# Kernel optimization log

Hardware: AMD Instinct MI355X
Metric: run time of the kernel (lower is better)

Reference implementation:

```python
import jax, jax.numpy as jnp
import numpy as np

T, D, E, K = 16384, 4096, 64, 8
GUMBEL_TAU = 1.0
ROUTER_TEMP = 1.0
SELECT_TEMP = None  # falls back to router_temp, as in the module
EPS = 1e-06


def setup_inputs() -> dict:
    key = jax.random.key(0)
    k1, k2, k3 = jax.random.split(key, 3)
    h = jax.random.normal(k1, (T, D), dtype=jnp.float32)
    # eqx.nn.Linear weight: shape (out_features, in_features), uniform init scale
    W = jax.random.normal(k2, (E, D), dtype=jnp.float32) * (1.0 / np.sqrt(D))
    # uniform noise for Gumbel, matching minval=1e-6, maxval=1-1e-6
    u = jax.random.uniform(k3, (T, E), minval=EPS, maxval=1.0 - EPS, dtype=jnp.float32)
    return {"h": h, "W": W, "u": u}


def reference(h, W, u):
    # logits_clean = vmap(Linear)(h) = h @ W.T, shape (T, E)
    logits_clean = jnp.einsum("td,ed->te", h, W)

    t_mix = jnp.clip(jnp.float32(ROUTER_TEMP), EPS, None)
    probs = jax.nn.softmax(logits_clean / t_mix, axis=-1)

    sel_temp = ROUTER_TEMP if SELECT_TEMP is None else SELECT_TEMP
    t_sel = jnp.clip(jnp.float32(sel_temp), EPS, None)
    logits_sel = logits_clean / t_sel

    # training path: Gumbel noise g = -log(-log(u))
    g = -jnp.log(-jnp.log(u))
    logits_sel = logits_sel + GUMBEL_TAU * g

    # hard top-k mask per row (scatter of ones at top-k indices == one_hot().sum())
    _, idx = jax.lax.top_k(logits_sel, K)  # (T, K)
    rows = jnp.arange(logits_sel.shape[0])[:, None]
    mask_full = jnp.zeros(logits_sel.shape, dtype=bool).at[rows, idx].set(True)

    return (mask_full, probs, logits_clean, logits_sel)
```

## Files before the change

### kernel.cpp

```cpp
#include <hip/hip_runtime.h>
#include <hip/hip_bf16.h>
#include <math.h>
#include <stdint.h>

#define T_ROWS 16384
#define D_DIM  4096
#define E_EXP  64
#define TOPK   8

constexpr float W_SCALE   = 64.0f;
constexpr float INV_SCALE = 1.0f / 64.0f;

constexpr int BM   = 64;
constexpr int BK   = 32;
constexpr int KQ   = D_DIM / 4;
constexpr int NIT  = KQ / BK;
constexpr int ABUF = 8192;
constexpr int BBUF = 8192;
constexpr int B_OFF = 3 * ABUF;
constexpr int LDS_TOT = B_OFF + 2 * BBUF;

typedef _Float16 f16x8 __attribute__((ext_vector_type(8)));
typedef __fp16   h16x2 __attribute__((ext_vector_type(2)));
typedef float    f32x4 __attribute__((ext_vector_type(4)));

__device__ __forceinline__ void gll16(const void* g, void* l) {
    __builtin_amdgcn_global_load_lds(
        (const __attribute__((address_space(1))) void*)g,
        (__attribute__((address_space(3))) void*)l, 16, 0, 0);
}
#define WAITV(n) asm volatile("s_waitcnt vmcnt(" #n ")" ::: "memory")
#define SB0()    __builtin_amdgcn_sched_barrier(0)

__global__ __launch_bounds__(256) void wprep_kernel(
    const float* __restrict__ W, _Float16* __restrict__ Wt)
{
    const int i  = blockIdx.x * 256 + threadIdx.x;
    const int e  = i >> 9;
    const int k8 = i & 511;
    const int k  = k8 << 3;
    const int t  = k >> 5;
    const int s  = (k >> 3) & 3;
    const float4 w0 = *(const float4*)&W[(size_t)e * D_DIM + k];
    const float4 w1 = *(const float4*)&W[(size_t)e * D_DIM + k + 4];
    const float xs[8] = {w0.x, w0.y, w0.z, w0.w, w1.x, w1.y, w1.z, w1.w};
    f16x8 hi, lo;
    #pragma unroll
    for (int j = 0; j < 8; ++j) {
        const float x = xs[j] * W_SCALE;
        const _Float16 hh = (_Float16)x;
        hi[j] = hh;
        lo[j] = (_Float16)(x - (float)hh);
    }
    const size_t o = (size_t)t * 4096 + e * 32 + ((s ^ (e & 3)) << 3);
    *(f16x8*)(Wt + o) = hi;
    *(f16x8*)(Wt + o + 2048) = lo;
}

__device__ __forceinline__ void cvt8(const float4 x0, const float4 x1,
                                     f16x8& hi, f16x8& lo) {
    const float xs[8] = {x0.x, x0.y, x0.z, x0.w, x1.x, x1.y, x1.z, x1.w};
    float hs[8], ls[8];
    #pragma unroll
    for (int j = 0; j < 8; ++j) {
        hs[j] = __uint_as_float(__float_as_uint(xs[j]) & 0xFFFFE000u);
        ls[j] = xs[j] - hs[j];
    }
    #pragma unroll
    for (int j = 0; j < 4; ++j) {
        const h16x2 ph = __builtin_amdgcn_cvt_pkrtz(hs[2 * j], hs[2 * j + 1]);
        const h16x2 pl = __builtin_amdgcn_cvt_pkrtz(ls[2 * j], ls[2 * j + 1]);
        hi[2 * j] = (_Float16)ph[0]; hi[2 * j + 1] = (_Float16)ph[1];
        lo[2 * j] = (_Float16)pl[0]; lo[2 * j + 1] = (_Float16)pl[1];
    }
}

__global__ __launch_bounds__(256, 4) void gemm_q_kernel(
    const float* __restrict__ h, const _Float16* __restrict__ Wt,
    float* __restrict__ out)
{
    __shared__ char smb[LDS_TOT];

    const int tid  = threadIdx.x;
    const int wv   = tid >> 6;
    const int lane = tid & 63;
    const int l15  = lane & 15;
    const int kg   = lane >> 4;
    const int wm   = wv >> 1;
    const int we   = wv & 1;
    const int row0 = blockIdx.x * BM;
    const int q    = blockIdx.y;
    const int kb   = q * KQ;

    const char* gA[2]; int lA[2];
    #pragma unroll
    for (int p = 0; p < 2; ++p) {
        const int row = wv * 16 + p * 8 + (lane >> 3);
        gA[p] = (const char*)h + ((size_t)(row0 + row) * D_DIM + kb) * 4
                + (((lane & 7) ^ (lane >> 3)) << 4);
        lA[p] = wv * 2048 + p * 1024;
    }
    const char* gB = (const char*)Wt + (size_t)(q * 32) * 8192
                     + wv * 2048 + lane * 16;
    const int lB = wv * 2048;

    int aro[2][2];
    #pragma unroll
    for (int f = 0; f < 2; ++f)
        #pragma unroll
        for (int qq = 0; qq < 2; ++qq)
            aro[f][qq] = (f * 32 + wm * 16 + l15) * 128
                       + (((kg * 2 + qq) ^ (l15 & 7)) << 4);
    int bro[2][2];
    #pragma unroll
    for (int sel = 0; sel < 2; ++sel)
        #pragma unroll
        for (int es = 0; es < 2; ++es) {
            const int e = we * 32 + es * 16 + l15;
            bro[sel][es] = sel * 4096 + e * 64 + ((kg ^ (e & 3)) << 4);
        }

    f32x4 acc[2][2] = {};
    float4 av[2][2];
    f16x8 bhf[2], blf[2];

    int aCur = 0, aNxt = ABUF, aStg = 2 * ABUF;

    #define STAGE_A(t, aAdd)                                          \
        { _Pragma("unroll")                                           \
          for (int p = 0; p < 2; ++p)                                 \
              gll16(gA[p] + (size_t)(t) * 128, smb + (aAdd) + lA[p]); }
    #define STAGE_B(t, par)                                           \
        { gll16(gB + (size_t)(t) * 8192,        smb + B_OFF + (par) * BBUF + lB); \
          gll16(gB + (size_t)(t) * 8192 + 1024, smb + B_OFF + (par) * BBUF + lB + 1024); }

    #define DSREAD(aAdd, par)                                                 \
        { _Pragma("unroll")                                                   \
          for (int f = 0; f < 2; ++f) {                                       \
              av[f][0] = *(const float4*)(smb + (aAdd) + aro[f][0]);          \
              av[f][1] = *(const float4*)(smb + (aAdd) + aro[f][1]);          \
          }                                                                   \
          _Pragma("unroll")                                                   \
          for (int es = 0; es < 2; ++es) {                                    \
              bhf[es] = *(const f16x8*)(smb + B_OFF + (par) * BBUF + bro[0][es]); \
              blf[es] = *(const f16x8*)(smb + B_OFF + (par) * BBUF + bro[1][es]); \
          } }

    #define MFMAS()                                                           \
        { f16x8 ah[2], al[2];                                                 \
          cvt8(av[0][0], av[0][1], ah[0], al[0]);                             \
          cvt8(av[1][0], av[1][1], ah[1], al[1]);                             \
          _Pragma("unroll")                                                   \
          for (int f = 0; f < 2; ++f)                                         \
              _Pragma("unroll")                                               \
              for (int es = 0; es < 2; ++es) {                                \
                  acc[f][es] = __builtin_amdgcn_mfma_f32_16x16x32_f16(ah[f], bhf[es], acc[f][es], 0, 0, 0); \
                  acc[f][es] = __builtin_amdgcn_mfma_f32_16x16x32_f16(ah[f], blf[es], acc[f][es], 0, 0, 0); \
                  acc[f][es] = __builtin_amdgcn_mfma_f32_16x16x32_f16(al[f], bhf[es], acc[f][es], 0, 0, 0); \
              } }

    #define ROT() { int t_ = aCur; aCur = aNxt; aNxt = aStg; aStg = t_; }

    STAGE_A(0, aCur)
    SB0();
    STAGE_B(0, 0)
    SB0();
    STAGE_A(1, aNxt)
    SB0();
    WAITV(2);
    SB0();
    __builtin_amdgcn_s_barrier();

    for (int i = 0; i < NIT - 2; ++i) {
        DSREAD(aCur, i & 1)
        STAGE_B(i + 1, (i + 1) & 1)
        SB0();
        STAGE_A(i + 2, aStg)
        SB0();
        __builtin_amdgcn_s_barrier();
        __builtin_amdgcn_s_setprio(1);
        MFMAS()
        __builtin_amdgcn_s_setprio(0);
        WAITV(2);
        SB0();
        __builtin_amdgcn_s_barrier();
        ROT();
    }
    DSREAD(aCur, (NIT - 2) & 1)
    STAGE_B(NIT - 1, (NIT - 1) & 1)
    SB0();
    __builtin_amdgcn_s_barrier();
    MFMAS()
    WAITV(0);
    SB0();
    __builtin_amdgcn_s_barrier();
    ROT();
    DSREAD(aCur, (NIT - 1) & 1)
    MFMAS()

    float* slot = out + (size_t)q * T_ROWS * E_EXP;
    #pragma unroll
    for (int f = 0; f < 2; ++f)
        #pragma unroll
        for (int es = 0; es < 2; ++es)
            #pragma unroll
            for (int r = 0; r < 4; ++r)
                slot[(size_t)(row0 + f * 32 + wm * 16 + kg * 4 + r) * E_EXP
                     + we * 32 + es * 16 + l15] = acc[f][es][r];
}

__global__ __launch_bounds__(256) void epilogue_kernel(
    const float* __restrict__ u, float* __restrict__ out)
{
    const int row  = blockIdx.x * 4 + (threadIdx.x >> 6);
    const int lane = threadIdx.x & 63;
    const size_t te = (size_t)T_ROWS * E_EXP;
    const size_t idx = (size_t)row * E_EXP + lane;

    const float p0 = out[0 * te + idx];
    const float p1 = out[1 * te + idx];
    const float p2 = out[2 * te + idx];
    const float p3 = out[3 * te + idx];
    const float val = (((p0 + p1) + p2) + p3) * INV_SCALE;

    out[2 * te + idx] = val;

    float m = val;
    #pragma unroll
    for (int off = 32; off; off >>= 1) m = fmaxf(m, __shfl_xor(m, off));
    const float p = expf(val - m);
    float ssum = p;
    #pragma unroll
    for (int off = 32; off; off >>= 1) ssum += __shfl_xor(ssum, off);
    out[1 * te + idx] = p / ssum;

    const float uv = u[idx];
    const float g = -logf(-logf(uv));
    const float sel = val + g;
    out[3 * te + idx] = sel;

    float v = sel;
    bool chosen = false;
    #pragma unroll
    for (int itk = 0; itk < TOPK; ++itk) {
        float mv = v;
        #pragma unroll
        for (int off = 32; off; off >>= 1) mv = fmaxf(mv, __shfl_xor(mv, off));
        const unsigned long long b = __ballot(v == mv);
        const int sl = __ffsll((long long)b) - 1;
        if (lane == sl) { chosen = true; v = -INFINITY; }
    }
    out[idx] = chosen ? 1.0f : 0.0f;
}

extern "C" void kernel_launch(void* const* d_in, const int* in_sizes, int n_in,
                              void* d_out, int out_size, void* d_ws, size_t ws_size,
                              hipStream_t stream) {
    const float* h = (const float*)d_in[0];
    const float* W = (const float*)d_in[1];
    const float* u = (const float*)d_in[2];
    float* out = (float*)d_out;

    _Float16* Wt = (_Float16*)d_ws;

    hipLaunchKernelGGL(wprep_kernel, dim3(E_EXP * D_DIM / 8 / 256), dim3(256),
                       0, stream, W, Wt);
    hipLaunchKernelGGL(gemm_q_kernel, dim3(T_ROWS / BM, 4), dim3(256),
                       0, stream, h, Wt, out);
    hipLaunchKernelGGL(epilogue_kernel, dim3(T_ROWS / 4), dim3(256),
                       0, stream, u, out);
}
```

Before: 79.02 us.

## Add dedicated producer wave for global-to-LDS loads in GEMM kernel

Splits the GEMM block into four consumer waves that only read LDS and issue MFMAs, plus a fifth producer wave that issues all global-to-LDS copies for A and B. The consumer loop loses its staging code and the barrier that sat between the LDS reads and the MFMAs. The aim is to take memory-issue and wait overhead off the compute waves so loads overlap with math. The cost is an extra wave per block and more block-wide barrier coupling. The requested 5 blocks per CU may not fit in LDS, and the single producer wave has to issue 16 loads per iteration, so it could become the bottleneck.

```diff
diff --git a/kernel.cpp b/kernel.cpp
--- a/kernel.cpp
+++ b/kernel.cpp
@@ -75,7 +75,7 @@
     }
 }
 
-__global__ __launch_bounds__(256, 4) void gemm_q_kernel(
+__global__ __launch_bounds__(320, 5) void gemm_q_kernel(
     const float* __restrict__ h, const _Float16* __restrict__ Wt,
     float* __restrict__ out)
 {
@@ -86,23 +86,59 @@
     const int lane = tid & 63;
     const int l15  = lane & 15;
     const int kg   = lane >> 4;
-    const int wm   = wv >> 1;
-    const int we   = wv & 1;
     const int row0 = blockIdx.x * BM;
     const int q    = blockIdx.y;
     const int kb   = q * KQ;
 
-    const char* gA[2]; int lA[2];
-    #pragma unroll
-    for (int p = 0; p < 2; ++p) {
-        const int row = wv * 16 + p * 8 + (lane >> 3);
-        gA[p] = (const char*)h + ((size_t)(row0 + row) * D_DIM + kb) * 4
-                + (((lane & 7) ^ (lane >> 3)) << 4);
-        lA[p] = wv * 2048 + p * 1024;
-    }
-    const char* gB = (const char*)Wt + (size_t)(q * 32) * 8192
-                     + wv * 2048 + lane * 16;
-    const int lB = wv * 2048;
+    int aCur = 0, aNxt = ABUF, aStg = 2 * ABUF;
+    #define ROT() { int t_ = aCur; aCur = aNxt; aNxt = aStg; aStg = t_; }
+
+    if (wv == 4) {
+        const char* gA0 = (const char*)h
+            + ((size_t)(row0 + (lane >> 3)) * D_DIM + kb) * 4
+            + (((lane & 7) ^ (lane >> 3)) << 4);
+        const char* gB0 = (const char*)Wt + (size_t)(q * 32) * 8192 + lane * 16;
+
+        #define P_STAGE_A(t, aAdd)                                            \
+            { _Pragma("unroll")                                               \
+              for (int j = 0; j < 8; ++j)                                     \
+                  gll16(gA0 + (size_t)j * 131072 + (size_t)(t) * 128,         \
+                        smb + (aAdd) + j * 1024); }
+        #define P_STAGE_B(t, par)                                             \
+            { _Pragma("unroll")                                               \
+              for (int j = 0; j < 8; ++j)                                     \
+                  gll16(gB0 + (size_t)(t) * 8192 + j * 1024,                  \
+                        smb + B_OFF + (par) * BBUF + j * 1024); }
+
+        P_STAGE_A(0, aCur)
+        SB0();
+        P_STAGE_B(0, 0)
+        SB0();
+        P_STAGE_A(1, aNxt)
+        SB0();
+        WAITV(8);
+        SB0();
+        __builtin_amdgcn_s_barrier();
+        for (int i = 0; i < NIT - 2; ++i) {
+            P_STAGE_B(i + 1, (i + 1) & 1)
+            SB0();
+            P_STAGE_A(i + 2, aStg)
+            SB0();
+            WAITV(8);
+            SB0();
+            __builtin_amdgcn_s_barrier();
+            ROT();
+        }
+        P_STAGE_B(NIT - 1, (NIT - 1) & 1)
+        SB0();
+        WAITV(0);
+        SB0();
+        __builtin_amdgcn_s_barrier();
+        return;
+    }
+
+    const int wm = wv >> 1;
+    const int we = wv & 1;
 
     int aro[2][2];
     #pragma unroll
@@ -123,16 +159,6 @@
     f32x4 acc[2][2] = {};
     float4 av[2][2];
     f16x8 bhf[2], blf[2];
-
-    int aCur = 0, aNxt = ABUF, aStg = 2 * ABUF;
-
-    #define STAGE_A(t, aAdd)                                          \
-        { _Pragma("unroll")                                           \
-          for (int p = 0; p < 2; ++p)                                 \
-              gll16(gA[p] + (size_t)(t) * 128, smb + (aAdd) + lA[p]); }
-    #define STAGE_B(t, par)                                           \
-        { gll16(gB + (size_t)(t) * 8192,        smb + B_OFF + (par) * BBUF + lB); \
-          gll16(gB + (size_t)(t) * 8192 + 1024, smb + B_OFF + (par) * BBUF + lB + 1024); }
 
     #define DSREAD(aAdd, par)                                                 \
         { _Pragma("unroll")                                                   \
@@ -159,40 +185,17 @@
                   acc[f][es] = __builtin_amdgcn_mfma_f32_16x16x32_f16(al[f], bhf[es], acc[f][es], 0, 0, 0); \
               } }
 
-    #define ROT() { int t_ = aCur; aCur = aNxt; aNxt = aStg; aStg = t_; }
-
-    STAGE_A(0, aCur)
-    SB0();
-    STAGE_B(0, 0)
-    SB0();
-    STAGE_A(1, aNxt)
-    SB0();
-    WAITV(2);
-    SB0();
     __builtin_amdgcn_s_barrier();
-
     for (int i = 0; i < NIT - 2; ++i) {
         DSREAD(aCur, i & 1)
-        STAGE_B(i + 1, (i + 1) & 1)
-        SB0();
-        STAGE_A(i + 2, aStg)
-        SB0();
-        __builtin_amdgcn_s_barrier();
         __builtin_amdgcn_s_setprio(1);
         MFMAS()
         __builtin_amdgcn_s_setprio(0);
-        WAITV(2);
-        SB0();
         __builtin_amdgcn_s_barrier();
         ROT();
     }
     DSREAD(aCur, (NIT - 2) & 1)
-    STAGE_B(NIT - 1, (NIT - 1) & 1)
-    SB0();
-    __builtin_amdgcn_s_barrier();
     MFMAS()
-    WAITV(0);
-    SB0();
     __builtin_amdgcn_s_barrier();
     ROT();
     DSREAD(aCur, (NIT - 1) & 1)
@@ -265,7 +268,7 @@
 
     hipLaunchKernelGGL(wprep_kernel, dim3(E_EXP * D_DIM / 8 / 256), dim3(256),
                        0, stream, W, Wt);
-    hipLaunchKernelGGL(gemm_q_kernel, dim3(T_ROWS / BM, 4), dim3(256),
+    hipLaunchKernelGGL(gemm_q_kernel, dim3(T_ROWS / BM, 4), dim3(320),
                        0, stream, h, Wt, out);
     hipLaunchKernelGGL(epilogue_kernel, dim3(T_ROWS / 4), dim3(256),
                        0, stream, u, out);
```

New measurement: 89.06 us. +12.7%, slower.
